# Kernel optimization log

Hardware: AMD Instinct MI355X
Metric: run time of the kernel (lower is better)

The kernel has to match this reference:

```python
import jax, jax.numpy as jnp
import numpy as np

SLOPE = 25.0   # fast_sigmoid surrogate slope (affects backward only)
THRESH = 1.0   # snntorch Leaky default threshold

@jax.custom_vjp
def spike(x):
    # Heaviside forward, fast-sigmoid surrogate backward
    return (x > 0).astype(x.dtype)

def _spike_fwd(x):
    return spike(x), x

def _spike_bwd(x, g):
    return (g / (SLOPE * jnp.abs(x) + 1.0) ** 2,)

spike.defvjp(_spike_fwd, _spike_bwd)


def setup_inputs() -> dict:
    key = jax.random.key(0)
    ks = jax.random.split(key, 16)
    B, T, F = 512, 1024, 64
    SNN, H, HOR = 128, 128, 24
    s = 0.05
    inp = {
        "x": jax.random.normal(ks[0], (B, T, F), jnp.float32),
        "proj_w": jax.random.normal(ks[1], (SNN, F), jnp.float32) * s,
        "proj_b": jnp.zeros((SNN,), jnp.float32),
        "beta1": jnp.full((SNN,), 0.9, jnp.float32),
        "beta2": jnp.full((SNN,), 0.9, jnp.float32),
        "gru_w_ih": jax.random.normal(ks[2], (3 * H, F + SNN), jnp.float32) * s,
        "gru_w_hh": jax.random.normal(ks[3], (3 * H, H), jnp.float32) * s,
        "gru_b_ih": jnp.zeros((3 * H,), jnp.float32),
        "gru_b_hh": jnp.zeros((3 * H,), jnp.float32),
        "attn_w1": jax.random.normal(ks[4], (H // 2, H), jnp.float32) * s,
        "attn_b1": jnp.zeros((H // 2,), jnp.float32),
        "attn_w2": jax.random.normal(ks[5], (1, H // 2), jnp.float32) * s,
        "attn_b2": jnp.zeros((1,), jnp.float32),
        "head_w": jax.random.normal(ks[6], (HOR, H), jnp.float32) * s,
        "head_b": jnp.zeros((HOR,), jnp.float32),
    }
    return inp


def reference(x, proj_w, proj_b, beta1, beta2,
              gru_w_ih, gru_w_hh, gru_b_ih, gru_b_hh,
              attn_w1, attn_b1, attn_w2, attn_b2, head_w, head_b):
    b1 = jnp.clip(beta1, 0.0, 0.99)
    b2 = jnp.clip(beta2, 0.0, 0.99)

    delta = x[:, 1:, :] - x[:, :-1, :]   # (B, T-1, F)
    raw = x[:, 1:, :]
    h_s = delta @ proj_w.T + proj_b      # (B, T-1, SNN)

    B = x.shape[0]
    SNN = proj_w.shape[0]

    # snntorch Leaky (subtract reset, reset from previous step's spike):
    # mem_t = beta*mem_{t-1} + in_t - spk_{t-1}*thr ; spk_t = H(mem_t - thr)
    def snn_step(carry, inp_t):
        m1, s1, m2, s2 = carry
        m1 = b1 * m1 + inp_t - s1 * THRESH
        s1n = spike(m1 - THRESH)
        m2 = b2 * m2 + s1n - s2 * THRESH
        s2n = spike(m2 - THRESH)
        return (m1, s1n, m2, s2n), m2

    z = jnp.zeros((B, SNN), x.dtype)
    _, mem_rec = jax.lax.scan(snn_step, (z, z, z, z), jnp.swapaxes(h_s, 0, 1))
    h_snn = jnp.swapaxes(mem_rec, 0, 1)             # (B, T-1, SNN)

    h_comb = jnp.concatenate([raw, h_snn], axis=-1)  # (B, T-1, F+SNN)

    # GRU (PyTorch gate layout: r, z, n)
    H = gru_w_hh.shape[1]
    x_proj = h_comb @ gru_w_ih.T + gru_b_ih          # (B, T-1, 3H)

    def gru_step(h, xp):
        gh = h @ gru_w_hh.T + gru_b_hh
        xr, xz, xn = jnp.split(xp, 3, axis=-1)
        hr, hz, hn = jnp.split(gh, 3, axis=-1)
        r = jax.nn.sigmoid(xr + hr)
        zg = jax.nn.sigmoid(xz + hz)
        n = jnp.tanh(xn + r * hn)
        h_new = (1.0 - zg) * n + zg * h
        return h_new, h_new

    h0 = jnp.zeros((B, H), x.dtype)
    _, gru_seq = jax.lax.scan(gru_step, h0, jnp.swapaxes(x_proj, 0, 1))
    gru_out = jnp.swapaxes(gru_seq, 0, 1)            # (B, T-1, H)

    # Temporal attention over time (dim=1)
    scores = jax.nn.relu(gru_out @ attn_w1.T + attn_b1) @ attn_w2.T + attn_b2  # (B, T-1, 1)
    w = jax.nn.softmax(scores, axis=1)
    h_ann = (w * gru_out).sum(axis=1)                # (B, H)

    return h_ann @ head_w.T + head_b                 # (B, horizon)
```

## Files before the change

kernel.cpp:

```cpp
#include <hip/hip_runtime.h>

typedef unsigned short u16;
typedef __attribute__((ext_vector_type(8))) short short8;
typedef __attribute__((ext_vector_type(4))) float f32x4;

__device__ __forceinline__ u16 f2bf(float f) {
  union { float f; unsigned u; } v; v.f = f;
  unsigned r = v.u + 0x7fffu + ((v.u >> 16) & 1u);
  return (u16)(r >> 16);
}
__device__ __forceinline__ u16 truncbf(float f) {
  union { float f; unsigned u; } v; v.f = f;
  return (u16)(v.u >> 16);
}
__device__ __forceinline__ float bf2f(u16 h) {
  union { unsigned u; float f; } v; v.u = ((unsigned)h) << 16;
  return v.f;
}
__device__ __forceinline__ void gll16(const void* g, void* l) {
  __builtin_amdgcn_global_load_lds((const __attribute__((address_space(1))) unsigned*)g,
                                   (__attribute__((address_space(3))) unsigned*)l, 16, 0, 0);
}

#define BATCH 512
#define TS 1023
#define NF 64
#define NS 128
#define NH 128
#define NG 384
#define NC 192
#define TCH 341

__global__ void k_prep(const float* __restrict__ wih, const float* __restrict__ w1,
                       u16* __restrict__ wihb, u16* __restrict__ w1b) {
  int i = blockIdx.x * 256 + threadIdx.x;
  if (i < NG * NC) wihb[i] = f2bf(wih[i]);
  if (i < 64 * NH) w1b[i] = f2bf(w1[i]);
}

__global__ __launch_bounds__(256) void k_front(const float* __restrict__ x,
                                               const float* __restrict__ pw,
                                               const float* __restrict__ pb,
                                               const float* __restrict__ beta1,
                                               const float* __restrict__ beta2,
                                               u16* __restrict__ hcomb) {
  __shared__ alignas(16) float xs[17 * 256];
  __shared__ alignas(16) u16 Ahi[64 * 64], Alo[64 * 64];
  __shared__ alignas(16) u16 Bhi[128 * 64], Blo[128 * 64];
  __shared__ float hst[64 * 138];
  const int tid = threadIdx.x, lane = tid & 63, w = tid >> 6;
  const int m16 = lane & 15, quad = lane >> 4;
  const int b = blockIdx.x;
  const float* xb = x + (long)b * 65536;

  #pragma unroll
  for (int j = 0; j < 4; ++j) {
    int cid = tid * 4 + j;
    int n = cid >> 3, ch = cid & 7;
    const float* src = pw + n * 64 + ch * 8;
    short8 h8, l8;
    #pragma unroll
    for (int jj = 0; jj < 8; ++jj) {
      float v = src[jj];
      u16 hh = truncbf(v);
      float l = v - bf2f(hh);
      h8[jj] = (short)hh; l8[jj] = (short)f2bf(l);
    }
    int chs = ch ^ (n & 7);
    *(short8*)(Bhi + n * 64 + chs * 8) = h8;
    *(short8*)(Blo + n * 64 + chs * 8) = l8;
  }
  float b1v = 0.f, b2v = 0.f, m1 = 0.f, s1 = 0.f, m2 = 0.f, s2 = 0.f;
  if (tid < 128) {
    b1v = fminf(fmaxf(beta1[tid], 0.f), 0.99f);
    b2v = fminf(fmaxf(beta2[tid], 0.f), 0.99f);
  }
  const int tm = (w >> 1) * 32, nn = (w & 1) * 64;
  float pbv[4];
  #pragma unroll
  for (int ni = 0; ni < 4; ++ni) pbv[ni] = pb[nn + ni * 16 + m16];

  for (int tile = 0; tile < 16; ++tile) {
    const int t0 = tile * 64;
    const int tl = (TS - t0 < 64) ? (TS - t0) : 64;
    const int rows = (1024 - t0 < 65) ? (1024 - t0) : 65;
    const int bytes = rows * 256;
    const int nch = (bytes + 1023) >> 10;
    for (int c = w; c < nch; c += 4) {
      int off = c * 1024 + lane * 16;
      if (off > bytes - 16) off = bytes - 16;
      gll16((const char*)xb + (long)t0 * 256 + off, (char*)xs + c * 1024);
    }
    __syncthreads();
    {
      int r = tid >> 2, kq = tid & 3;
      const float* x0 = xs + r * 64 + kq * 16;
      short8 h8[2], l8[2];
      #pragma unroll
      for (int cc = 0; cc < 2; ++cc)
        #pragma unroll
        for (int jj = 0; jj < 8; ++jj) {
          float d = x0[64 + cc * 8 + jj] - x0[cc * 8 + jj];
          u16 hh = truncbf(d);
          float l = d - bf2f(hh);
          h8[cc][jj] = (short)hh; l8[cc][jj] = (short)f2bf(l);
        }
      #pragma unroll
      for (int cc = 0; cc < 2; ++cc) {
        int chs = (kq * 2 + cc) ^ (r & 7);
        *(short8*)(Ahi + r * 64 + chs * 8) = h8[cc];
        *(short8*)(Alo + r * 64 + chs * 8) = l8[cc];
      }
    }
    __syncthreads();
    f32x4 acc[2][4] = {};
    #pragma unroll
    for (int kc = 0; kc < 2; ++kc) {
      short8 ah[2], al[2], bh[4], bl[4];
      #pragma unroll
      for (int mi = 0; mi < 2; ++mi) {
        int row = tm + mi * 16 + m16;
        int chs = (kc * 4 + quad) ^ (row & 7);
        ah[mi] = *(const short8*)(Ahi + row * 64 + chs * 8);
        al[mi] = *(const short8*)(Alo + row * 64 + chs * 8);
      }
      #pragma unroll
      for (int ni = 0; ni < 4; ++ni) {
        int row = nn + ni * 16 + m16;
        int chs = (kc * 4 + quad) ^ (row & 7);
        bh[ni] = *(const short8*)(Bhi + row * 64 + chs * 8);
        bl[ni] = *(const short8*)(Blo + row * 64 + chs * 8);
      }
      #pragma unroll
      for (int mi = 0; mi < 2; ++mi)
        #pragma unroll
        for (int ni = 0; ni < 4; ++ni) {
          acc[mi][ni] = __builtin_amdgcn_mfma_f32_16x16x32_bf16(ah[mi], bh[ni], acc[mi][ni], 0, 0, 0);
          acc[mi][ni] = __builtin_amdgcn_mfma_f32_16x16x32_bf16(ah[mi], bl[ni], acc[mi][ni], 0, 0, 0);
          acc[mi][ni] = __builtin_amdgcn_mfma_f32_16x16x32_bf16(al[mi], bh[ni], acc[mi][ni], 0, 0, 0);
        }
    }
    #pragma unroll
    for (int mi = 0; mi < 2; ++mi)
      #pragma unroll
      for (int ni = 0; ni < 4; ++ni)
        #pragma unroll
        for (int rr = 0; rr < 4; ++rr)
          hst[(tm + mi * 16 + quad * 4 + rr) * 138 + nn + ni * 16 + m16] = acc[mi][ni][rr] + pbv[ni];
    __syncthreads();
    if (tid < 128) {
      const int n = tid;
      u16* dst = hcomb + ((long)t0 * 512 + b) * NC + 64 + n;
      for (int tt = 0; tt < tl; tt += 8) {
        float v[8];
        #pragma unroll
        for (int jj = 0; jj < 8; ++jj) {
          int t = tt + jj; if (t > 63) t = 63;
          v[jj] = hst[t * 138 + n];
        }
        #pragma unroll
        for (int jj = 0; jj < 8; ++jj) {
          int t = tt + jj;
          if (t < tl) {
            m1 = b1v * m1 + v[jj] - s1;
            s1 = (m1 > 1.0f) ? 1.0f : 0.0f;
            m2 = b2v * m2 + s1 - s2;
            s2 = (m2 > 1.0f) ? 1.0f : 0.0f;
            dst[(long)t * (512 * NC)] = f2bf(m2);
          }
        }
      }
    } else {
      const int f = tid & 63, half = (tid >> 6) & 1;
      for (int r = half; r < tl; r += 2)
        hcomb[((long)(t0 + r) * 512 + b) * NC + f] = f2bf(xs[(r + 1) * 64 + f]);
    }
    __syncthreads();
  }
}

__global__ __launch_bounds__(256) void k_xproj(const u16* __restrict__ hc, const u16* __restrict__ wih,
                                               const float* __restrict__ bih, u16* __restrict__ xp) {
  __shared__ alignas(16) u16 As[4096], Bs[4096];
  const int tid = threadIdx.x, lane = tid & 63, w = tid >> 6;
  const int m16 = lane & 15, quad = lane >> 4;
  const long row0 = (long)blockIdx.x * 128;
  const int n0 = blockIdx.y * 128;
  const int wm = (w >> 1) * 64, wn = (w & 1) * 64;
  f32x4 acc[4][4] = {};
  const char* gA = (const char*)hc + (row0 + (lane >> 2)) * (NC * 2) + (lane & 3) * 16;
  const char* gB = (const char*)wih + (long)(n0 + (lane >> 2)) * (NC * 2) + (lane & 3) * 16;
  for (int kc = 0; kc < 6; ++kc) {
    #pragma unroll
    for (int i = 0; i < 2; ++i) {
      int q = i * 4 + w;
      gll16(gA + (long)q * 16 * (NC * 2) + kc * 64, (char*)As + q * 1024);
      gll16(gB + (long)q * 16 * (NC * 2) + kc * 64, (char*)Bs + q * 1024);
    }
    __syncthreads();
    short8 af[4], bfr[4];
    #pragma unroll
    for (int mi = 0; mi < 4; ++mi) af[mi] = *(const short8*)((const char*)As + (wm + mi * 16 + m16) * 64 + quad * 16);
    #pragma unroll
    for (int ni = 0; ni < 4; ++ni) bfr[ni] = *(const short8*)((const char*)Bs + (wn + ni * 16 + m16) * 64 + quad * 16);
    #pragma unroll
    for (int mi = 0; mi < 4; ++mi)
      #pragma unroll
      for (int ni = 0; ni < 4; ++ni)
        acc[mi][ni] = __builtin_amdgcn_mfma_f32_16x16x32_bf16(af[mi], bfr[ni], acc[mi][ni], 0, 0, 0);
    __syncthreads();
  }
  #pragma unroll
  for (int ni = 0; ni < 4; ++ni) {
    int n = n0 + wn + ni * 16 + m16;
    float bias = bih[n];
    #pragma unroll
    for (int mi = 0; mi < 4; ++mi) {
      long r = row0 + wm + mi * 16 + quad * 4;
      #pragma unroll
      for (int rr = 0; rr < 4; ++rr)
        xp[(r + rr) * NG + n] = f2bf(acc[mi][ni][rr] + bias);
    }
  }
}

__global__ __launch_bounds__(256, 1) void k_gru(const u16* __restrict__ xp, const float* __restrict__ whh,
                                                const float* __restrict__ bhh, u16* __restrict__ gout,
                                                float* __restrict__ h_state, int first) {
  __shared__ alignas(16) u16 frag[2 * 2048];
  const int tid = threadIdx.x, lane = tid & 63, w = tid >> 6;
  const int m16 = lane & 15, quad = lane >> 4;
  const long bg0 = (long)blockIdx.x * 2;
  {
    short8 z8 = {};
    *(short8*)((char*)frag + tid * 16) = z8;
    *(short8*)((char*)frag + 4096 + tid * 16) = z8;
  }
  short8 wf[6][4];
  #pragma unroll
  for (int g = 0; g < 3; ++g)
    #pragma unroll
    for (int hh = 0; hh < 2; ++hh)
      #pragma unroll
      for (int c = 0; c < 4; ++c) {
        const float* src = whh + (long)(g * 128 + 32 * w + hh * 16 + m16) * NH + c * 32 + quad * 8;
        short8 v;
        #pragma unroll
        for (int jj = 0; jj < 8; ++jj) v[jj] = (short)f2bf(src[jj]);
        wf[g * 2 + hh][c] = v;
      }
  const int bq = quad & 1, hq = quad >> 1;
  const int j = 32 * w + hq * 16 + m16;
  const long brow = bg0 + bq;
  const float br_ = bhh[j], bz_ = bhh[128 + j], bn_ = bhh[256 + j];
  float h = first ? 0.f : h_state[brow * NH + j];
  const int fragoff = w * 1024 + 64 * bq + 256 * (hq * 2 + (m16 >> 3)) + 2 * (m16 & 7);
  __syncthreads();
  {
    u16 hb0 = f2bf(h);
    *(u16*)((char*)frag + fragoff) = hb0;
    *(u16*)((char*)frag + fragoff + 128) = hb0;
  }
  const u16* xbase = xp + brow * NG + j;
  u16 pr[8], pz[8], pn[8], sbuf[8];
  #pragma unroll
  for (int u = 0; u < 8; ++u) {
    const u16* xr = xbase + (long)u * (512 * NG);
    pr[u] = xr[0]; pz[u] = xr[128]; pn[u] = xr[256];
  }
  __syncthreads();

#define GRU_STEP(T, U)                                                                     \
  {                                                                                        \
    const int cur = ((T) & 1) * 4096, nxt = 4096 - cur;                                    \
    short8 af[4];                                                                          \
    _Pragma("unroll")                                                                      \
    for (int c = 0; c < 4; ++c)                                                            \
      af[c] = *(const short8*)((const char*)frag + cur + c * 1024 + lane * 16);            \
    f32x4 zero = {0.f, 0.f, 0.f, 0.f};                                                     \
    f32x4 accA[6], accB[6];                                                                \
    _Pragma("unroll")                                                                      \
    for (int nt = 0; nt < 6; ++nt) {                                                       \
      accA[nt] = __builtin_amdgcn_mfma_f32_16x16x32_bf16(af[0], wf[nt][0], zero, 0, 0, 0); \
      accB[nt] = __builtin_amdgcn_mfma_f32_16x16x32_bf16(af[2], wf[nt][2], zero, 0, 0, 0); \
    }                                                                                      \
    _Pragma("unroll")                                                                      \
    for (int nt = 0; nt < 6; ++nt) {                                                       \
      accA[nt] = __builtin_amdgcn_mfma_f32_16x16x32_bf16(af[1], wf[nt][1], accA[nt], 0, 0, 0); \
      accB[nt] = __builtin_amdgcn_mfma_f32_16x16x32_bf16(af[3], wf[nt][3], accB[nt], 0, 0, 0); \
    }                                                                                      \
    float ghr = (hq ? (accA[1][0] + accB[1][0]) : (accA[0][0] + accB[0][0])) + br_;        \
    float ghz = (hq ? (accA[3][0] + accB[3][0]) : (accA[2][0] + accB[2][0])) + bz_;        \
    float ghn = (hq ? (accA[5][0] + accB[5][0]) : (accA[4][0] + accB[4][0])) + bn_;        \
    float xrv = bf2f(pr[U]), xzv = bf2f(pz[U]), xnv = bf2f(pn[U]);                         \
    float rg = 1.f / (1.f + __expf(-(xrv + ghr)));                                         \
    float zg = 1.f / (1.f + __expf(-(xzv + ghz)));                                         \
    float niv = xnv + rg * ghn;                                                            \
    float ng = 1.f - 2.f / (1.f + __expf(2.f * niv));                                      \
    h = (1.f - zg) * ng + zg * h;                                                          \
    u16 hb = f2bf(h);                                                                      \
    sbuf[U] = hb;                                                                          \
    *(u16*)((char*)frag + nxt + fragoff) = hb;                                             \
    *(u16*)((char*)frag + nxt + fragoff + 128) = hb;                                       \
    __syncthreads();                                                                       \
  }

  for (int t8 = 0; t8 < 336; t8 += 8) {
    if (t8 > 0) {
      #pragma unroll
      for (int u = 0; u < 8; ++u)
        gout[((long)(t8 - 8 + u) * 512 + brow) * NH + j] = sbuf[u];
    }
    u16 npr[8], npz[8], npn[8];
    #pragma unroll
    for (int u = 0; u < 8; ++u) {
      long tp = t8 + 8 + u; if (tp > TCH - 1) tp = TCH - 1;
      const u16* xr = xbase + tp * (512 * NG);
      npr[u] = xr[0]; npz[u] = xr[128]; npn[u] = xr[256];
    }
    GRU_STEP(t8 + 0, 0) GRU_STEP(t8 + 1, 1) GRU_STEP(t8 + 2, 2) GRU_STEP(t8 + 3, 3)
    GRU_STEP(t8 + 4, 4) GRU_STEP(t8 + 5, 5) GRU_STEP(t8 + 6, 6) GRU_STEP(t8 + 7, 7)
    #pragma unroll
    for (int u = 0; u < 8; ++u) { pr[u] = npr[u]; pz[u] = npz[u]; pn[u] = npn[u]; }
  }
  #pragma unroll
  for (int u = 0; u < 8; ++u)
    gout[((long)(328 + u) * 512 + brow) * NH + j] = sbuf[u];
  #pragma unroll
  for (int u = 0; u < 5; ++u) {
    GRU_STEP(336 + u, u)
    gout[((long)(336 + u) * 512 + brow) * NH + j] = sbuf[u];
  }
#undef GRU_STEP
  h_state[brow * NH + j] = h;
}

__global__ __launch_bounds__(256) void k_score(const u16* __restrict__ gbf, const u16* __restrict__ w1,
                                               const float* __restrict__ b1, const float* __restrict__ w2,
                                               const float* __restrict__ b2, float* __restrict__ scores) {
  __shared__ alignas(16) u16 Gs[4096], Ws[2048];
  const int tid = threadIdx.x, lane = tid & 63, w = tid >> 6;
  const int m16 = lane & 15, quad = lane >> 4;
  const long row0 = (long)blockIdx.x * 128;
  f32x4 acc[2][4] = {};
  const char* gG = (const char*)gbf + (row0 + (lane >> 2)) * (NH * 2) + (lane & 3) * 16;
  const char* gW = (const char*)w1 + (long)(w * 16 + (lane >> 2)) * (NH * 2) + (lane & 3) * 16;
  for (int kc = 0; kc < 4; ++kc) {
    #pragma unroll
    for (int i = 0; i < 2; ++i) {
      int q = i * 4 + w;
      gll16(gG + (long)q * 16 * (NH * 2) + kc * 64, (char*)Gs + q * 1024);
    }
    gll16(gW + kc * 64, (char*)Ws + w * 1024);
    __syncthreads();
    short8 af[2], bfr[4];
    #pragma unroll
    for (int mi = 0; mi < 2; ++mi) af[mi] = *(const short8*)((const char*)Gs + (w * 32 + mi * 16 + m16) * 64 + quad * 16);
    #pragma unroll
    for (int ni = 0; ni < 4; ++ni) bfr[ni] = *(const short8*)((const char*)Ws + (ni * 16 + m16) * 64 + quad * 16);
    #pragma unroll
    for (int mi = 0; mi < 2; ++mi)
      #pragma unroll
      for (int ni = 0; ni < 4; ++ni)
        acc[mi][ni] = __builtin_amdgcn_mfma_f32_16x16x32_bf16(af[mi], bfr[ni], acc[mi][ni], 0, 0, 0);
    __syncthreads();
  }
  float b2v = b2[0];
  float w2v[4], b1v[4];
  #pragma unroll
  for (int ni = 0; ni < 4; ++ni) { w2v[ni] = w2[ni * 16 + m16]; b1v[ni] = b1[ni * 16 + m16]; }
  #pragma unroll
  for (int mi = 0; mi < 2; ++mi) {
    #pragma unroll
    for (int rr = 0; rr < 4; ++rr) {
      float v = 0.f;
      #pragma unroll
      for (int ni = 0; ni < 4; ++ni) {
        float hv = acc[mi][ni][rr] + b1v[ni];
        hv = hv > 0.f ? hv : 0.f;
        v = fmaf(hv, w2v[ni], v);
      }
      v += __shfl_xor(v, 1, 64); v += __shfl_xor(v, 2, 64);
      v += __shfl_xor(v, 4, 64); v += __shfl_xor(v, 8, 64);
      if (m16 == 0) scores[row0 + w * 32 + mi * 16 + quad * 4 + rr] = v + b2v;
    }
  }
}

__global__ __launch_bounds__(256) void k_attn(const float* __restrict__ scores, const u16* __restrict__ gout,
                                              const float* __restrict__ headw, const float* __restrict__ headb,
                                              float* __restrict__ out) {
  __shared__ float sc[TS];
  __shared__ float red[8];
  __shared__ float part[8][132];
  __shared__ float hann[128];
  const int tid = threadIdx.x, lane = tid & 63, w = tid >> 6;
  const long b = blockIdx.x;
  const float* srow = scores + b;
  float s0[4];
  #pragma unroll
  for (int i = 0; i < 4; ++i) {
    int t = tid + i * 256;
    s0[i] = (t < TS) ? srow[(long)t * 512] : -1e30f;
  }
  float mx = fmaxf(fmaxf(s0[0], s0[1]), fmaxf(s0[2], s0[3]));
  #pragma unroll
  for (int off = 32; off > 0; off >>= 1) mx = fmaxf(mx, __shfl_xor(mx, off, 64));
  if (lane == 0) red[w] = mx;
  __syncthreads();
  mx = fmaxf(fmaxf(red[0], red[1]), fmaxf(red[2], red[3]));
  float sum = 0.f;
  #pragma unroll
  for (int i = 0; i < 4; ++i) {
    int t = tid + i * 256;
    if (t < TS) { float e = __expf(s0[i] - mx); sc[t] = e; sum += e; }
  }
  #pragma unroll
  for (int off = 32; off > 0; off >>= 1) sum += __shfl_xor(sum, off, 64);
  if (lane == 0) red[4 + w] = sum;
  __syncthreads();
  float inv = 1.f / (red[4] + red[5] + red[6] + red[7]);
  const int jg = tid & 31, sl = tid >> 5;
  float acc[4] = {0.f, 0.f, 0.f, 0.f};
  const u16* gbase = gout + b * NH + jg * 4;
  for (int t = sl; t < TS; t += 8) {
    float wt = sc[t];
    ushort4 g4 = *(const ushort4*)(gbase + (long)t * (512 * NH));
    acc[0] = fmaf(wt, bf2f(g4.x), acc[0]);
    acc[1] = fmaf(wt, bf2f(g4.y), acc[1]);
    acc[2] = fmaf(wt, bf2f(g4.z), acc[2]);
    acc[3] = fmaf(wt, bf2f(g4.w), acc[3]);
  }
  #pragma unroll
  for (int i = 0; i < 4; ++i) part[sl][jg * 4 + i] = acc[i];
  __syncthreads();
  if (tid < 128) {
    float v = 0.f;
    #pragma unroll
    for (int s = 0; s < 8; ++s) v += part[s][tid];
    hann[tid] = v * inv;
  }
  __syncthreads();
  if (tid < 24) {
    float a = headb[tid];
    const float* hwr = headw + tid * 128;
    for (int k = 0; k < 128; k += 4) {
      float4 h4 = *(const float4*)&hann[k];
      float4 w4 = *(const float4*)&hwr[k];
      a = fmaf(h4.x, w4.x, a); a = fmaf(h4.y, w4.y, a);
      a = fmaf(h4.z, w4.z, a); a = fmaf(h4.w, w4.w, a);
    }
    out[b * 24 + tid] = a;
  }
}

extern "C" void kernel_launch(void* const* d_in, const int* in_sizes, int n_in,
                              void* d_out, int out_size, void* d_ws, size_t ws_size,
                              hipStream_t stream) {
  const float* x      = (const float*)d_in[0];
  const float* proj_w = (const float*)d_in[1];
  const float* proj_b = (const float*)d_in[2];
  const float* beta1  = (const float*)d_in[3];
  const float* beta2  = (const float*)d_in[4];
  const float* gwih   = (const float*)d_in[5];
  const float* gwhh   = (const float*)d_in[6];
  const float* gbih   = (const float*)d_in[7];
  const float* gbhh   = (const float*)d_in[8];
  const float* aw1    = (const float*)d_in[9];
  const float* ab1    = (const float*)d_in[10];
  const float* aw2    = (const float*)d_in[11];
  const float* ab2    = (const float*)d_in[12];
  const float* hw     = (const float*)d_in[13];
  const float* hb     = (const float*)d_in[14];
  float* out = (float*)d_out;
  char* ws = (char*)d_ws;

  u16*   hcomb  = (u16*)(ws);
  u16*   xpbuf  = (u16*)(ws + 201129984L);
  u16*   gru    = (u16*)(ws + 335216640L);
  float* scores = (float*)(ws + 469303296L);
  u16*   wihb   = (u16*)(ws + 471398400L);
  u16*   w1b    = (u16*)(ws + 471545856L);
  float* hstate = (float*)(ws + 471562240L);

  k_prep<<<288, 256, 0, stream>>>(gwih, aw1, wihb, w1b);
  k_front<<<512, 256, 0, stream>>>(x, proj_w, proj_b, beta1, beta2, hcomb);
  for (int c = 0; c < 3; ++c) {
    long rowbase = (long)c * TCH * 512;
    k_xproj<<<dim3(1364, 3), 256, 0, stream>>>(hcomb + rowbase * NC, wihb, gbih, xpbuf);
    k_gru<<<256, 256, 0, stream>>>(xpbuf, gwhh, gbhh, gru + rowbase * NH, hstate, c == 0 ? 1 : 0);
  }
  k_score<<<4092, 256, 0, stream>>>(gru, w1b, ab1, aw2, ab2, scores);
  k_attn<<<512, 256, 0, stream>>>(scores, gru, hw, hb, out);
}
```

Measured before the change: 1.125 ms.

## Load front-end MFMA operands directly from global into registers, dropping LDS staging

The front kernel stops staging x tiles and the split hi/lo projection weights in shared memory. The weight fragments are now converted once into registers, and the delta operands are read straight from global memory per MFMA fragment. Two barriers per tile go away, LDS use shrinks, and launch bounds now request two blocks per CU for more occupancy. In exchange, x is read redundantly from global (each row twice, plus the raw copy path), and register pressure rises from the 16 resident weight fragments.

```diff
diff --git a/kernel.cpp b/kernel.cpp
--- a/kernel.cpp
+++ b/kernel.cpp
@@ -38,44 +38,42 @@
   if (i < 64 * NH) w1b[i] = f2bf(w1[i]);
 }
 
-__global__ __launch_bounds__(256) void k_front(const float* __restrict__ x,
-                                               const float* __restrict__ pw,
-                                               const float* __restrict__ pb,
-                                               const float* __restrict__ beta1,
-                                               const float* __restrict__ beta2,
-                                               u16* __restrict__ hcomb) {
-  __shared__ alignas(16) float xs[17 * 256];
-  __shared__ alignas(16) u16 Ahi[64 * 64], Alo[64 * 64];
-  __shared__ alignas(16) u16 Bhi[128 * 64], Blo[128 * 64];
+__global__ __launch_bounds__(256, 2) void k_front(const float* __restrict__ x,
+                                                  const float* __restrict__ pw,
+                                                  const float* __restrict__ pb,
+                                                  const float* __restrict__ beta1,
+                                                  const float* __restrict__ beta2,
+                                                  u16* __restrict__ hcomb) {
   __shared__ float hst[64 * 138];
   const int tid = threadIdx.x, lane = tid & 63, w = tid >> 6;
   const int m16 = lane & 15, quad = lane >> 4;
   const int b = blockIdx.x;
   const float* xb = x + (long)b * 65536;
 
-  #pragma unroll
-  for (int j = 0; j < 4; ++j) {
-    int cid = tid * 4 + j;
-    int n = cid >> 3, ch = cid & 7;
-    const float* src = pw + n * 64 + ch * 8;
-    short8 h8, l8;
-    #pragma unroll
-    for (int jj = 0; jj < 8; ++jj) {
-      float v = src[jj];
-      u16 hh = truncbf(v);
-      float l = v - bf2f(hh);
-      h8[jj] = (short)hh; l8[jj] = (short)f2bf(l);
-    }
-    int chs = ch ^ (n & 7);
-    *(short8*)(Bhi + n * 64 + chs * 8) = h8;
-    *(short8*)(Blo + n * 64 + chs * 8) = l8;
-  }
+  const int tm = (w >> 1) * 32, nn = (w & 1) * 64;
+
+  short8 bh[2][4], bl[2][4];
+  #pragma unroll
+  for (int kc = 0; kc < 2; ++kc)
+    #pragma unroll
+    for (int ni = 0; ni < 4; ++ni) {
+      const float* src = pw + (nn + ni * 16 + m16) * 64 + kc * 32 + quad * 8;
+      f32x4 v0 = *(const f32x4*)src;
+      f32x4 v1 = *(const f32x4*)(src + 4);
+      #pragma unroll
+      for (int jj = 0; jj < 8; ++jj) {
+        float v = (jj < 4) ? v0[jj & 3] : v1[jj & 3];
+        u16 hh = truncbf(v);
+        bh[kc][ni][jj] = (short)hh;
+        bl[kc][ni][jj] = (short)f2bf(v - bf2f(hh));
+      }
+    }
+
   float b1v = 0.f, b2v = 0.f, m1 = 0.f, s1 = 0.f, m2 = 0.f, s2 = 0.f;
   if (tid < 128) {
     b1v = fminf(fmaxf(beta1[tid], 0.f), 0.99f);
     b2v = fminf(fmaxf(beta2[tid], 0.f), 0.99f);
   }
-  const int tm = (w >> 1) * 32, nn = (w & 1) * 64;
   float pbv[4];
   #pragma unroll
   for (int ni = 0; ni < 4; ++ni) pbv[ni] = pb[nn + ni * 16 + m16];
@@ -83,61 +81,37 @@
   for (int tile = 0; tile < 16; ++tile) {
     const int t0 = tile * 64;
     const int tl = (TS - t0 < 64) ? (TS - t0) : 64;
-    const int rows = (1024 - t0 < 65) ? (1024 - t0) : 65;
-    const int bytes = rows * 256;
-    const int nch = (bytes + 1023) >> 10;
-    for (int c = w; c < nch; c += 4) {
-      int off = c * 1024 + lane * 16;
-      if (off > bytes - 16) off = bytes - 16;
-      gll16((const char*)xb + (long)t0 * 256 + off, (char*)xs + c * 1024);
-    }
-    __syncthreads();
-    {
-      int r = tid >> 2, kq = tid & 3;
-      const float* x0 = xs + r * 64 + kq * 16;
-      short8 h8[2], l8[2];
-      #pragma unroll
-      for (int cc = 0; cc < 2; ++cc)
-        #pragma unroll
-        for (int jj = 0; jj < 8; ++jj) {
-          float d = x0[64 + cc * 8 + jj] - x0[cc * 8 + jj];
-          u16 hh = truncbf(d);
-          float l = d - bf2f(hh);
-          h8[cc][jj] = (short)hh; l8[cc][jj] = (short)f2bf(l);
-        }
-      #pragma unroll
-      for (int cc = 0; cc < 2; ++cc) {
-        int chs = (kq * 2 + cc) ^ (r & 7);
-        *(short8*)(Ahi + r * 64 + chs * 8) = h8[cc];
-        *(short8*)(Alo + r * 64 + chs * 8) = l8[cc];
-      }
-    }
-    __syncthreads();
+
     f32x4 acc[2][4] = {};
     #pragma unroll
     for (int kc = 0; kc < 2; ++kc) {
-      short8 ah[2], al[2], bh[4], bl[4];
+      short8 ah[2], al[2];
       #pragma unroll
       for (int mi = 0; mi < 2; ++mi) {
         int row = tm + mi * 16 + m16;
-        int chs = (kc * 4 + quad) ^ (row & 7);
-        ah[mi] = *(const short8*)(Ahi + row * 64 + chs * 8);
-        al[mi] = *(const short8*)(Alo + row * 64 + chs * 8);
+        int tA = t0 + row; if (tA > 1022) tA = 1022;
+        const float* p0 = xb + (long)tA * 64 + kc * 32 + quad * 8;
+        f32x4 lo0 = *(const f32x4*)p0;
+        f32x4 lo1 = *(const f32x4*)(p0 + 4);
+        f32x4 hi0 = *(const f32x4*)(p0 + 64);
+        f32x4 hi1 = *(const f32x4*)(p0 + 68);
+        float d[8];
+        #pragma unroll
+        for (int jj = 0; jj < 4; ++jj) { d[jj] = hi0[jj] - lo0[jj]; d[4 + jj] = hi1[jj] - lo1[jj]; }
+        #pragma unroll
+        for (int jj = 0; jj < 8; ++jj) {
+          u16 hh = truncbf(d[jj]);
+          ah[mi][jj] = (short)hh;
+          al[mi][jj] = (short)f2bf(d[jj] - bf2f(hh));
+        }
       }
       #pragma unroll
-      for (int ni = 0; ni < 4; ++ni) {
-        int row = nn + ni * 16 + m16;
-        int chs = (kc * 4 + quad) ^ (row & 7);
-        bh[ni] = *(const short8*)(Bhi + row * 64 + chs * 8);
-        bl[ni] = *(const short8*)(Blo + row * 64 + chs * 8);
-      }
-      #pragma unroll
       for (int mi = 0; mi < 2; ++mi)
         #pragma unroll
         for (int ni = 0; ni < 4; ++ni) {
-          acc[mi][ni] = __builtin_amdgcn_mfma_f32_16x16x32_bf16(ah[mi], bh[ni], acc[mi][ni], 0, 0, 0);
-          acc[mi][ni] = __builtin_amdgcn_mfma_f32_16x16x32_bf16(ah[mi], bl[ni], acc[mi][ni], 0, 0, 0);
-          acc[mi][ni] = __builtin_amdgcn_mfma_f32_16x16x32_bf16(al[mi], bh[ni], acc[mi][ni], 0, 0, 0);
+          acc[mi][ni] = __builtin_amdgcn_mfma_f32_16x16x32_bf16(ah[mi], bh[kc][ni], acc[mi][ni], 0, 0, 0);
+          acc[mi][ni] = __builtin_amdgcn_mfma_f32_16x16x32_bf16(ah[mi], bl[kc][ni], acc[mi][ni], 0, 0, 0);
+          acc[mi][ni] = __builtin_amdgcn_mfma_f32_16x16x32_bf16(al[mi], bh[kc][ni], acc[mi][ni], 0, 0, 0);
         }
     }
     #pragma unroll
@@ -173,7 +147,7 @@
     } else {
       const int f = tid & 63, half = (tid >> 6) & 1;
       for (int r = half; r < tl; r += 2)
-        hcomb[((long)(t0 + r) * 512 + b) * NC + f] = f2bf(xs[(r + 1) * 64 + f]);
+        hcomb[((long)(t0 + r) * 512 + b) * NC + f] = f2bf(xb[(long)(t0 + r + 1) * 64 + f]);
     }
     __syncthreads();
   }
```

After: 1.075 ms. 1.05x faster.
